# Kernel tuning notes

Measured on AMD Instinct MI355X. Metric: run time of the kernel, lower is better.

## Reference

```python
import jax, jax.numpy as jnp
import numpy as np

B, OBS, H, N = 16384, 512, 1024, 9

def setup_inputs() -> dict:
    key = jax.random.key(0)
    ks = jax.random.split(key, 12)
    s = 0.02
    return {
        "obs": jax.random.normal(ks[0], (B, OBS), jnp.float32),
        "agent_positions": jax.random.normal(ks[1], (B, N, 3), jnp.float32),
        "W1": jax.random.normal(ks[2], (OBS, H), jnp.float32) * s,
        "b1": jnp.zeros((H,), jnp.float32),
        "W2": jax.random.normal(ks[3], (H, H), jnp.float32) * s,
        "b2": jnp.zeros((H,), jnp.float32),
        "Wc1": jax.random.normal(ks[4], (H, H // 2), jnp.float32) * s,
        "bc1": jnp.zeros((H // 2,), jnp.float32),
        "Wc2": jax.random.normal(ks[5], (H // 2, 1), jnp.float32) * s,
        "bc2": jnp.zeros((1,), jnp.float32),
        "Wt1": jax.random.normal(ks[6], (H, H // 2), jnp.float32) * s,
        "bt1": jnp.zeros((H // 2,), jnp.float32),
        "Wt2": jax.random.normal(ks[7], (H // 2, 1), jnp.float32) * s,
        "bt2": jnp.zeros((1,), jnp.float32),
        "Wk1": jax.random.normal(ks[8], (2 * H, H), jnp.float32) * s,
        "bk1": jnp.zeros((H,), jnp.float32),
        "Wk2": jax.random.normal(ks[9], (H, 1), jnp.float32) * s,
        "bk2": jnp.zeros((1,), jnp.float32),
    }


def reference(obs, agent_positions, W1, b1, W2, b2, Wc1, bc1, Wc2, bc2,
              Wt1, bt1, Wt2, bt2, Wk1, bk1, Wk2, bk2):
    # global features: Linear->ReLU->Linear->ReLU
    g = jax.nn.relu(obs @ W1 + b1)
    g = jax.nn.relu(g @ W2 + b2)  # [B, H]

    # Each per-agent head is applied to the SAME g in the original loop,
    # so one pass + broadcast is mathematically identical.
    cov = jax.nn.sigmoid(jax.nn.relu(g @ Wc1 + bc1) @ Wc2 + bc2)  # [B,1]
    trk = jax.nn.sigmoid(jax.nn.relu(g @ Wt1 + bt1) @ Wt2 + bt2)  # [B,1]
    coop_in = jnp.concatenate([g, g], axis=-1)                    # [B,2H]
    coop = jax.nn.sigmoid(jax.nn.relu(coop_in @ Wk1 + bk1) @ Wk2 + bk2)  # [B,1]
    # mean over 8 identical cooperation scores == the score itself

    coverage = jnp.broadcast_to(cov, (cov.shape[0], N))      # [B, N]
    tracking = jnp.broadcast_to(trk, (trk.shape[0], N))      # [B, N]
    cooperation = jnp.broadcast_to(coop, (coop.shape[0], N)) # [B, N]
    return (coverage, tracking, cooperation)
```

## Files before the change

kernel.cpp:

```cpp
#include <hip/hip_runtime.h>
#include <hip/hip_bf16.h>

#define B_ROWS 16384
#define OBS_D  512
#define H_D    1024
#define N_AG   9

typedef __attribute__((ext_vector_type(8))) short short8;
typedef __attribute__((ext_vector_type(4))) float floatx4;

__device__ __forceinline__ unsigned short f_to_bf_raw(float f) {
  union { float f; unsigned u; } c; c.f = f;
  unsigned u = c.u;
  u = u + 0x7FFF + ((u >> 16) & 1);
  return (unsigned short)(u >> 16);
}

__device__ __forceinline__ size_t frag_off(int n, int k, int KT32) {
  const int ft = (n >> 4) * KT32 + (k >> 5);
  const int ln = (n & 15) | (((k >> 3) & 3) << 4);
  return ((size_t)ft * 64 + ln) * 8 + (k & 7);
}

__global__ __launch_bounds__(256) void prep_all(
    const float* __restrict__ obs,
    const float* __restrict__ W1, const float* __restrict__ W2,
    const float* __restrict__ Wc1, const float* __restrict__ Wt1,
    const float* __restrict__ Wk1,
    const float* __restrict__ bc1, const float* __restrict__ bt1,
    const float* __restrict__ bk1,
    const float* __restrict__ Wc2, const float* __restrict__ Wt2,
    const float* __restrict__ Wk2,
    unsigned short* __restrict__ obs_bf,
    unsigned short* __restrict__ W1f, unsigned short* __restrict__ W2f,
    unsigned short* __restrict__ WHf,
    float* __restrict__ bias2048, float* __restrict__ w2cat) {
  __shared__ float t[32][33];
  const int bx  = blockIdx.x;
  const int tid = threadIdx.x;

  if (bx < 4096) {
    int i = (bx * 256 + tid) * 8;
    float4 a = *(const float4*)(obs + i);
    float4 b = *(const float4*)(obs + i + 4);
    short8 o;
    o[0] = (short)f_to_bf_raw(a.x); o[1] = (short)f_to_bf_raw(a.y);
    o[2] = (short)f_to_bf_raw(a.z); o[3] = (short)f_to_bf_raw(a.w);
    o[4] = (short)f_to_bf_raw(b.x); o[5] = (short)f_to_bf_raw(b.y);
    o[6] = (short)f_to_bf_raw(b.z); o[7] = (short)f_to_bf_raw(b.w);
    *(short8*)(obs_bf + i) = o;
    return;
  }

  const int tx = tid & 31;
  const int ty = tid >> 5;

  if (bx < 4608) {
    const int tt = bx - 4096;
    const int k0 = (tt & 15) * 32;
    const int n0 = (tt >> 4) * 32;
#pragma unroll
    for (int i = ty; i < 32; i += 8)
      t[i][tx] = W1[(size_t)(k0 + i) * 1024 + n0 + tx];
    __syncthreads();
#pragma unroll
    for (int i = ty; i < 32; i += 8)
      W1f[frag_off(n0 + i, k0 + tx, 16)] = f_to_bf_raw(t[tx][i]);
    return;
  }

  if (bx < 5632) {
    const int tt = bx - 4608;
    const int k0 = (tt & 31) * 32;
    const int n0 = (tt >> 5) * 32;
#pragma unroll
    for (int i = ty; i < 32; i += 8)
      t[i][tx] = W2[(size_t)(k0 + i) * 1024 + n0 + tx];
    __syncthreads();
#pragma unroll
    for (int i = ty; i < 32; i += 8)
      W2f[frag_off(n0 + i, k0 + tx, 32)] = f_to_bf_raw(t[tx][i]);
    return;
  }

  if (bx < 7680) {
    const int tt = bx - 5632;
    const int k0 = (tt & 31) * 32;
    const int n0 = (tt >> 5) * 32;
#pragma unroll
    for (int i = ty; i < 32; i += 8) {
      const int n = n0 + tx;
      float v;
      if (n0 < 512)
        v = Wc1[(size_t)(k0 + i) * 512 + n];
      else if (n0 < 1024)
        v = Wt1[(size_t)(k0 + i) * 512 + (n - 512)];
      else
        v = Wk1[(size_t)(k0 + i) * 1024 + (n - 1024)]
          + Wk1[(size_t)(k0 + i + 1024) * 1024 + (n - 1024)];
      t[i][tx] = v;
    }
    __syncthreads();
#pragma unroll
    for (int i = ty; i < 32; i += 8)
      WHf[frag_off(n0 + i, k0 + tx, 32)] = f_to_bf_raw(t[tx][i]);
    return;
  }

  {
    int n = (bx - 7680) * 256 + tid;
    float b, w;
    if (n < 512)       { b = bc1[n];        w = Wc2[n]; }
    else if (n < 1024) { b = bt1[n - 512];  w = Wt2[n - 512]; }
    else               { b = bk1[n - 1024]; w = Wk2[n - 1024]; }
    bias2048[n] = b;
    w2cat[n] = w;
  }
}

#define GLD_LDS(gp, lp)                                                        \
  __builtin_amdgcn_global_load_lds(                                            \
      (const __attribute__((address_space(1))) void*)(gp),                     \
      (__attribute__((address_space(3))) void*)(lp), 16, 0, 0)

#define SCB __builtin_amdgcn_sched_barrier(0)

#define MFMA_BF16(a, b, c) __builtin_amdgcn_mfma_f32_16x16x32_bf16(a, b, c, 0, 0, 0)

#define ST_A(T, kh)                                                            \
  GLD_LDS(gA0 + (size_t)(T) * 128 + (kh) * 64,                                 \
          Lds + ((T) & 1) * 65536 + (kh) * 16384 + lA0);                       \
  GLD_LDS(gA1 + (size_t)(T) * 128 + (kh) * 64,                                 \
          Lds + ((T) & 1) * 65536 + (kh) * 16384 + lA0 + 8192)

#define ST_B(T, kh)                                                            \
  GLD_LDS(gB0 + (size_t)(2 * (T) + (kh)) * 1024,                               \
          Lds + ((T) & 1) * 65536 + (kh) * 16384 + lB0);                       \
  GLD_LDS(gB1 + (size_t)(2 * (T) + (kh)) * 1024,                               \
          Lds + ((T) & 1) * 65536 + (kh) * 16384 + lB0 + 8192)

#define FB4(pb)                                                                \
  Fb[0] = *(const short8*)((pb) + fbB);                                        \
  Fb[1] = *(const short8*)((pb) + fbB + 1024);                                 \
  Fb[2] = *(const short8*)((pb) + fbB + 2048);                                 \
  Fb[3] = *(const short8*)((pb) + fbB + 3072)

#define MFMA16(mh)                                                             \
  acc[(mh)*4+0][0] = MFMA_BF16(Fa0, Fb[0], acc[(mh)*4+0][0]);                  \
  acc[(mh)*4+0][1] = MFMA_BF16(Fa0, Fb[1], acc[(mh)*4+0][1]);                  \
  acc[(mh)*4+0][2] = MFMA_BF16(Fa0, Fb[2], acc[(mh)*4+0][2]);                  \
  acc[(mh)*4+0][3] = MFMA_BF16(Fa0, Fb[3], acc[(mh)*4+0][3]);                  \
  acc[(mh)*4+1][0] = MFMA_BF16(Fa1, Fb[0], acc[(mh)*4+1][0]);                  \
  acc[(mh)*4+1][1] = MFMA_BF16(Fa1, Fb[1], acc[(mh)*4+1][1]);                  \
  acc[(mh)*4+1][2] = MFMA_BF16(Fa1, Fb[2], acc[(mh)*4+1][2]);                  \
  acc[(mh)*4+1][3] = MFMA_BF16(Fa1, Fb[3], acc[(mh)*4+1][3]);                  \
  acc[(mh)*4+2][0] = MFMA_BF16(Fa2, Fb[0], acc[(mh)*4+2][0]);                  \
  acc[(mh)*4+2][1] = MFMA_BF16(Fa2, Fb[1], acc[(mh)*4+2][1]);                  \
  acc[(mh)*4+2][2] = MFMA_BF16(Fa2, Fb[2], acc[(mh)*4+2][2]);                  \
  acc[(mh)*4+2][3] = MFMA_BF16(Fa2, Fb[3], acc[(mh)*4+2][3]);                  \
  acc[(mh)*4+3][0] = MFMA_BF16(Fa3, Fb[0], acc[(mh)*4+3][0]);                  \
  acc[(mh)*4+3][1] = MFMA_BF16(Fa3, Fb[1], acc[(mh)*4+3][1]);                  \
  acc[(mh)*4+3][2] = MFMA_BF16(Fa3, Fb[2], acc[(mh)*4+3][2]);                  \
  acc[(mh)*4+3][3] = MFMA_BF16(Fa3, Fb[3], acc[(mh)*4+3][3])

#define PHASE(TT, ks, mh, EXTRA_READS, STAGE_STMT, PRE_BAR2)                   \
  {                                                                            \
    const char* pb = Lds + ((TT) & 1) * 65536 + (ks) * 16384;                  \
    short8 Fa0 = *(const short8*)(pb + faB + ((mh)*4+0)*1024);                 \
    short8 Fa1 = *(const short8*)(pb + faB + ((mh)*4+1)*1024);                 \
    short8 Fa2 = *(const short8*)(pb + faB + ((mh)*4+2)*1024);                 \
    short8 Fa3 = *(const short8*)(pb + faB + ((mh)*4+3)*1024);                 \
    EXTRA_READS;                                                               \
    STAGE_STMT;                                                                \
    SCB; __builtin_amdgcn_s_barrier(); SCB;                                    \
    __builtin_amdgcn_s_setprio(1);                                             \
    MFMA16(mh);                                                                \
    __builtin_amdgcn_s_setprio(0);                                             \
    PRE_BAR2;                                                                  \
    SCB; __builtin_amdgcn_s_barrier(); SCB;                                    \
  }

#define GEMM_CORE_V13(ACC_DECL)                                                \
  __shared__ __align__(16) char Lds[131072];                                   \
  const int tid  = threadIdx.x;                                                \
  const int lane = tid & 63;                                                   \
  const int wave = tid >> 6;                                         \
  const int m0 = blockIdx.x * 256;                                             \
  const int n0 = blockIdx.y * 256;                                             \
  const int wm = (wave & 1) * 128;                  \
  const int wn = (wave >> 1) * 64;                                             \
  const int fr = lane & 15;                                                    \
  const int fq = lane >> 4;                                                    \
  ACC_DECL;                                                                    \
  constexpr int KT   = K >> 6;                                                 \
  constexpr int KT32 = K >> 5;                                                 \
  const size_t rowb = (size_t)K * 2;                                           \
    \
    \
   \
  const char* gA0 = (const char*)A                                             \
      + (size_t)(m0 + wave * 16 + (lane >> 2)) * rowb                          \
      + (((lane & 3) ^ ((lane >> 3) & 3)) * 16);                               \
  const char* gA1 = gA0 + (size_t)128 * rowb;                                  \
  const char* gB0 = (const char*)Bf                                            \
      + ((size_t)((n0 >> 4) + wave) * KT32) * 1024 + lane * 16;                \
  const char* gB1 = gB0 + (size_t)8 * KT32 * 1024;                             \
  const int lA0 = wave * 1024 + lane * 16;                                     \
  const int lB0 = 32768 + wave * 1024 + lane * 16;                             \
       \
  const int faB = (wm + fr) * 64 + ((fq ^ ((fr >> 1) & 3)) * 16);              \
  const int fbB = 32768 + ((wave >> 1) * 4) * 1024 + lane * 16;                \
  short8 Fb[4];                                                                \
              \
  ST_A(0, 0); ST_B(0, 0); ST_A(0, 1); ST_B(0, 1);                              \
  SCB;                                                                         \
  ST_A(1, 0); ST_B(1, 0);                                                      \
  SCB;                                                                         \
  asm volatile("s_waitcnt vmcnt(4)" ::: "memory");       \
  __builtin_amdgcn_s_barrier();                  \
  SCB;                                                                         \
  _Pragma("unroll")                                                            \
  for (int T = 0; T < KT; ++T) {           \
    PHASE(T, 0, 0, FB4(pb), if (T + 1 < KT) { ST_A(T + 1, 1); }, (void)0);     \
    PHASE(T, 0, 1, (void)0, if (T + 1 < KT) { ST_B(T + 1, 1); }, (void)0);     \
    PHASE(T, 1, 0, FB4(pb), if (T + 2 < KT) { ST_A(T + 2, 0); }, (void)0);     \
    PHASE(T, 1, 1, (void)0, if (T + 2 < KT) { ST_B(T + 2, 0); },               \
          if (T + 1 < KT) {                                                    \
            SCB;                                                               \
            if (T + 2 < KT) {                                                  \
              asm volatile("s_waitcnt vmcnt(4)" ::: "memory");                 \
            } else {                                                           \
              asm volatile("s_waitcnt vmcnt(0)" ::: "memory");                 \
            }                                                                  \
            SCB;                                                               \
          });                                                                  \
  }

#define ACC_INIT                                                               \
  floatx4 acc[8][4];                                                           \
  _Pragma("unroll")                                                            \
  for (int i = 0; i < 8; ++i)                                                  \
    _Pragma("unroll")                                                          \
    for (int j = 0; j < 4; ++j) acc[i][j] = (floatx4){0.f, 0.f, 0.f, 0.f}

template <int K>
__global__ __launch_bounds__(512, 2) void gemm_bias_relu(
    const unsigned short* __restrict__ A,
    const unsigned short* __restrict__ Bf,
    const float* __restrict__ bias,
    unsigned short* __restrict__ C,
    int M, int N) {
  GEMM_CORE_V13(ACC_INIT)

#pragma unroll
  for (int ni = 0; ni < 4; ++ni) {
    const int gn = n0 + wn + ni * 16 + fr;
    const float bv = bias[gn];
#pragma unroll
    for (int mi = 0; mi < 8; ++mi) {
#pragma unroll
      for (int r = 0; r < 4; ++r) {
        const int gm = m0 + wm + mi * 16 + fq * 4 + r;
        float v = acc[mi][ni][r] + bv;
        v = v > 0.f ? v : 0.f;
        C[(size_t)gm * N + gn] = f_to_bf_raw(v);
      }
    }
  }
}

template <int K>
__global__ __launch_bounds__(512, 2) void gemm_heads_fused(
    const unsigned short* __restrict__ A,
    const unsigned short* __restrict__ Bf,
    const float* __restrict__ bias,
    const float* __restrict__ w2,
    float* __restrict__ part,
    int M, int N) {
  GEMM_CORE_V13(ACC_INIT)

  const int j = blockIdx.y * 4 + (wave >> 1);
  float w2v[4], bv[4];
#pragma unroll
  for (int ni = 0; ni < 4; ++ni) {
    const int gn = n0 + wn + ni * 16 + fr;
    w2v[ni] = w2[gn];
    bv[ni]  = bias[gn];
  }
#pragma unroll
  for (int mi = 0; mi < 8; ++mi) {
#pragma unroll
    for (int r = 0; r < 4; ++r) {
      float p = 0.f;
#pragma unroll
      for (int ni = 0; ni < 4; ++ni) {
        float v = acc[mi][ni][r] + bv[ni];
        v = v > 0.f ? v : 0.f;
        p += v * w2v[ni];
      }
      p += __shfl_xor(p, 1);
      p += __shfl_xor(p, 2);
      p += __shfl_xor(p, 4);
      p += __shfl_xor(p, 8);
      if (fr == 0) {
        const int gm = m0 + wm + mi * 16 + fq * 4 + r;
        part[(size_t)j * B_ROWS + gm] = p;
      }
    }
  }
}

__global__ __launch_bounds__(256) void final_out(
    const float* __restrict__ part,
    const float* __restrict__ bc2, const float* __restrict__ bt2,
    const float* __restrict__ bk2, float* __restrict__ out) {
  const int row = blockIdx.x * 256 + threadIdx.x;
  float sc = 0.f, st = 0.f, sk = 0.f;
#pragma unroll
  for (int j = 0; j < 8; ++j)  sc += part[(size_t)j * B_ROWS + row];
#pragma unroll
  for (int j = 8; j < 16; ++j) st += part[(size_t)j * B_ROWS + row];
#pragma unroll
  for (int j = 16; j < 32; ++j) sk += part[(size_t)j * B_ROWS + row];
  const float cv = 1.f / (1.f + expf(-(sc + bc2[0])));
  const float tv = 1.f / (1.f + expf(-(st + bt2[0])));
  const float kv = 1.f / (1.f + expf(-(sk + bk2[0])));
  float* o0 = out + (size_t)row * N_AG;
  float* o1 = out + (size_t)(B_ROWS + row) * N_AG;
  float* o2 = out + (size_t)(2 * B_ROWS + row) * N_AG;
#pragma unroll
  for (int a = 0; a < N_AG; ++a) { o0[a] = cv; o1[a] = tv; o2[a] = kv; }
}

extern "C" void kernel_launch(void* const* d_in, const int* in_sizes, int n_in,
                              void* d_out, int out_size, void* d_ws, size_t ws_size,
                              hipStream_t stream) {
  const float* obs = (const float*)d_in[0];
  const float* W1  = (const float*)d_in[2];
  const float* b1  = (const float*)d_in[3];
  const float* W2  = (const float*)d_in[4];
  const float* b2  = (const float*)d_in[5];
  const float* Wc1 = (const float*)d_in[6];
  const float* bc1 = (const float*)d_in[7];
  const float* Wc2 = (const float*)d_in[8];
  const float* bc2 = (const float*)d_in[9];
  const float* Wt1 = (const float*)d_in[10];
  const float* bt1 = (const float*)d_in[11];
  const float* Wt2 = (const float*)d_in[12];
  const float* bt2 = (const float*)d_in[13];
  const float* Wk1 = (const float*)d_in[14];
  const float* bk1 = (const float*)d_in[15];
  const float* Wk2 = (const float*)d_in[16];
  const float* bk2 = (const float*)d_in[17];
  float* out = (float*)d_out;

  char* ws = (char*)d_ws;
  const size_t MB = 1024 * 1024;
  const size_t FULL_NEED = 70 * MB + 16 * 1024;

  unsigned short *obs_bf, *W1f, *W2f, *WHf, *G1, *G;
  float *bias2048, *w2cat, *PART;
  const bool full = (ws_size == 0) || (ws_size >= FULL_NEED);

  if (full) {
    obs_bf   = (unsigned short*)(ws + 0);
    W1f      = (unsigned short*)(ws + 16 * MB);
    G        = (unsigned short*)(ws + 0);
    G1       = (unsigned short*)(ws + 32 * MB);
    PART     = (float*)(ws + 32 * MB);
    W2f      = (unsigned short*)(ws + 64 * MB);
    WHf      = (unsigned short*)(ws + 66 * MB);
    bias2048 = (float*)(ws + 70 * MB);
    w2cat    = (float*)(ws + 70 * MB + 8 * 1024);
  } else {
    obs_bf   = (unsigned short*)(ws + 0);
    G1       = (unsigned short*)(ws + 16 * MB);
    G        = (unsigned short*)(ws + 32 * MB);
    W1f      = (unsigned short*)(ws + 48 * MB);
    W2f      = (unsigned short*)(ws + 49 * MB);
    WHf      = (unsigned short*)(ws + 51 * MB);
    bias2048 = (float*)(ws + 55 * MB);
    w2cat    = (float*)(ws + 55 * MB + 8 * 1024);
    PART     = (float*)(ws + 55 * MB + 16 * 1024);
  }

  prep_all<<<7688, 256, 0, stream>>>(obs, W1, W2, Wc1, Wt1, Wk1,
                                     bc1, bt1, bk1, Wc2, Wt2, Wk2,
                                     obs_bf, W1f, W2f, WHf, bias2048, w2cat);

  if (full) {
    gemm_bias_relu<512><<<dim3(64, 4), 512, 0, stream>>>(
        obs_bf, W1f, b1, G1, B_ROWS, 1024);
    gemm_bias_relu<1024><<<dim3(64, 4), 512, 0, stream>>>(
        G1, W2f, b2, G, B_ROWS, 1024);
    gemm_heads_fused<1024><<<dim3(64, 8), 512, 0, stream>>>(
        G, WHf, bias2048, w2cat, PART, B_ROWS, 2048);
  } else {
    for (int h = 0; h < 2; ++h) {
      const size_t ro = (size_t)h * 8192;
      gemm_bias_relu<512><<<dim3(32, 4), 512, 0, stream>>>(
          obs_bf + ro * 512, W1f, b1, G1, 8192, 1024);
      gemm_bias_relu<1024><<<dim3(32, 4), 512, 0, stream>>>(
          G1, W2f, b2, G, 8192, 1024);
      gemm_heads_fused<1024><<<dim3(32, 8), 512, 0, stream>>>(
          G, WHf, bias2048, w2cat, PART + ro, 8192, 2048);
    }
  }

  final_out<<<B_ROWS / 256, 256, 0, stream>>>(PART, bc2, bt2, bk2, out);
}
```

Measured before the change: 251.8 us.

## Load B fragments directly from global into registers, halve LDS footprint

The weight operand B is no longer staged through LDS. Each wave now reads its pre-swizzled B fragments straight from global memory into registers, double-buffered across k-halves. LDS shrinks from 128KB to 64KB and holds only the A tiles, which cuts LDS write/read traffic and could allow more occupancy. The cost is redundant global/L2 reads of B by the two waves that share the same N columns, and exposed global latency on the B loads. The vmcnt accounting also changes and now mixes register loads with LDS DMA loads.

```diff
diff --git a/kernel.cpp b/kernel.cpp
--- a/kernel.cpp
+++ b/kernel.cpp
@@ -127,61 +127,54 @@
 
 #define MFMA_BF16(a, b, c) __builtin_amdgcn_mfma_f32_16x16x32_bf16(a, b, c, 0, 0, 0)
 
-#define ST_A(T, kh)                                                            \
+#define ST_A14(T, kh)                                                          \
   GLD_LDS(gA0 + (size_t)(T) * 128 + (kh) * 64,                                 \
-          Lds + ((T) & 1) * 65536 + (kh) * 16384 + lA0);                       \
+          Lds + ((T) & 1) * 32768 + (kh) * 16384 + lA0);                       \
   GLD_LDS(gA1 + (size_t)(T) * 128 + (kh) * 64,                                 \
-          Lds + ((T) & 1) * 65536 + (kh) * 16384 + lA0 + 8192)
-
-#define ST_B(T, kh)                                                            \
-  GLD_LDS(gB0 + (size_t)(2 * (T) + (kh)) * 1024,                               \
-          Lds + ((T) & 1) * 65536 + (kh) * 16384 + lB0);                       \
-  GLD_LDS(gB1 + (size_t)(2 * (T) + (kh)) * 1024,                               \
-          Lds + ((T) & 1) * 65536 + (kh) * 16384 + lB0 + 8192)
-
-#define FB4(pb)                                                                \
-  Fb[0] = *(const short8*)((pb) + fbB);                                        \
-  Fb[1] = *(const short8*)((pb) + fbB + 1024);                                 \
-  Fb[2] = *(const short8*)((pb) + fbB + 2048);                                 \
-  Fb[3] = *(const short8*)((pb) + fbB + 3072)
-
-#define MFMA16(mh)                                                             \
-  acc[(mh)*4+0][0] = MFMA_BF16(Fa0, Fb[0], acc[(mh)*4+0][0]);                  \
-  acc[(mh)*4+0][1] = MFMA_BF16(Fa0, Fb[1], acc[(mh)*4+0][1]);                  \
-  acc[(mh)*4+0][2] = MFMA_BF16(Fa0, Fb[2], acc[(mh)*4+0][2]);                  \
-  acc[(mh)*4+0][3] = MFMA_BF16(Fa0, Fb[3], acc[(mh)*4+0][3]);                  \
-  acc[(mh)*4+1][0] = MFMA_BF16(Fa1, Fb[0], acc[(mh)*4+1][0]);                  \
-  acc[(mh)*4+1][1] = MFMA_BF16(Fa1, Fb[1], acc[(mh)*4+1][1]);                  \
-  acc[(mh)*4+1][2] = MFMA_BF16(Fa1, Fb[2], acc[(mh)*4+1][2]);                  \
-  acc[(mh)*4+1][3] = MFMA_BF16(Fa1, Fb[3], acc[(mh)*4+1][3]);                  \
-  acc[(mh)*4+2][0] = MFMA_BF16(Fa2, Fb[0], acc[(mh)*4+2][0]);                  \
-  acc[(mh)*4+2][1] = MFMA_BF16(Fa2, Fb[1], acc[(mh)*4+2][1]);                  \
-  acc[(mh)*4+2][2] = MFMA_BF16(Fa2, Fb[2], acc[(mh)*4+2][2]);                  \
-  acc[(mh)*4+2][3] = MFMA_BF16(Fa2, Fb[3], acc[(mh)*4+2][3]);                  \
-  acc[(mh)*4+3][0] = MFMA_BF16(Fa3, Fb[0], acc[(mh)*4+3][0]);                  \
-  acc[(mh)*4+3][1] = MFMA_BF16(Fa3, Fb[1], acc[(mh)*4+3][1]);                  \
-  acc[(mh)*4+3][2] = MFMA_BF16(Fa3, Fb[2], acc[(mh)*4+3][2]);                  \
-  acc[(mh)*4+3][3] = MFMA_BF16(Fa3, Fb[3], acc[(mh)*4+3][3])
-
-#define PHASE(TT, ks, mh, EXTRA_READS, STAGE_STMT, PRE_BAR2)                   \
+          Lds + ((T) & 1) * 32768 + (kh) * 16384 + lA0 + 8192)
+
+#define LDB(dst, T2, s)                                                        \
+  dst[0] = *(const short8*)(gB + ((size_t)0 * KT32 + 2 * (T2) + (s)) * 512);   \
+  dst[1] = *(const short8*)(gB + ((size_t)1 * KT32 + 2 * (T2) + (s)) * 512);   \
+  dst[2] = *(const short8*)(gB + ((size_t)2 * KT32 + 2 * (T2) + (s)) * 512);   \
+  dst[3] = *(const short8*)(gB + ((size_t)3 * KT32 + 2 * (T2) + (s)) * 512)
+
+#define MFMA16F(mh, FB)                                                        \
+  acc[(mh)*4+0][0] = MFMA_BF16(Fa0, FB[0], acc[(mh)*4+0][0]);                  \
+  acc[(mh)*4+0][1] = MFMA_BF16(Fa0, FB[1], acc[(mh)*4+0][1]);                  \
+  acc[(mh)*4+0][2] = MFMA_BF16(Fa0, FB[2], acc[(mh)*4+0][2]);                  \
+  acc[(mh)*4+0][3] = MFMA_BF16(Fa0, FB[3], acc[(mh)*4+0][3]);                  \
+  acc[(mh)*4+1][0] = MFMA_BF16(Fa1, FB[0], acc[(mh)*4+1][0]);                  \
+  acc[(mh)*4+1][1] = MFMA_BF16(Fa1, FB[1], acc[(mh)*4+1][1]);                  \
+  acc[(mh)*4+1][2] = MFMA_BF16(Fa1, FB[2], acc[(mh)*4+1][2]);                  \
+  acc[(mh)*4+1][3] = MFMA_BF16(Fa1, FB[3], acc[(mh)*4+1][3]);                  \
+  acc[(mh)*4+2][0] = MFMA_BF16(Fa2, FB[0], acc[(mh)*4+2][0]);                  \
+  acc[(mh)*4+2][1] = MFMA_BF16(Fa2, FB[1], acc[(mh)*4+2][1]);                  \
+  acc[(mh)*4+2][2] = MFMA_BF16(Fa2, FB[2], acc[(mh)*4+2][2]);                  \
+  acc[(mh)*4+2][3] = MFMA_BF16(Fa2, FB[3], acc[(mh)*4+2][3]);                  \
+  acc[(mh)*4+3][0] = MFMA_BF16(Fa3, FB[0], acc[(mh)*4+3][0]);                  \
+  acc[(mh)*4+3][1] = MFMA_BF16(Fa3, FB[1], acc[(mh)*4+3][1]);                  \
+  acc[(mh)*4+3][2] = MFMA_BF16(Fa3, FB[2], acc[(mh)*4+3][2]);                  \
+  acc[(mh)*4+3][3] = MFMA_BF16(Fa3, FB[3], acc[(mh)*4+3][3])
+
+#define PHASE14(TT, ks, mh, FB, EXTRA, PRE_BAR2)                               \
   {                                                                            \
-    const char* pb = Lds + ((TT) & 1) * 65536 + (ks) * 16384;                  \
+    const char* pb = Lds + ((TT) & 1) * 32768 + (ks) * 16384;                  \
     short8 Fa0 = *(const short8*)(pb + faB + ((mh)*4+0)*1024);                 \
     short8 Fa1 = *(const short8*)(pb + faB + ((mh)*4+1)*1024);                 \
     short8 Fa2 = *(const short8*)(pb + faB + ((mh)*4+2)*1024);                 \
     short8 Fa3 = *(const short8*)(pb + faB + ((mh)*4+3)*1024);                 \
-    EXTRA_READS;                                                               \
-    STAGE_STMT;                                                                \
+    EXTRA;                                                                     \
     SCB; __builtin_amdgcn_s_barrier(); SCB;                                    \
     __builtin_amdgcn_s_setprio(1);                                             \
-    MFMA16(mh);                                                                \
+    MFMA16F(mh, FB);                                                           \
     __builtin_amdgcn_s_setprio(0);                                             \
     PRE_BAR2;                                                                  \
     SCB; __builtin_amdgcn_s_barrier(); SCB;                                    \
   }
 
-#define GEMM_CORE_V13(ACC_DECL)                                                \
-  __shared__ __align__(16) char Lds[131072];                                   \
+#define GEMM_CORE_V14(ACC_DECL)                                                \
+  __shared__ __align__(16) char Lds[65536];                                    \
   const int tid  = threadIdx.x;                                                \
   const int lane = tid & 63;                                                   \
   const int wave = tid >> 6;                                         \
@@ -195,45 +188,43 @@
   constexpr int KT   = K >> 6;                                                 \
   constexpr int KT32 = K >> 5;                                                 \
   const size_t rowb = (size_t)K * 2;                                           \
-    \
-    \
-   \
+          \
   const char* gA0 = (const char*)A                                             \
       + (size_t)(m0 + wave * 16 + (lane >> 2)) * rowb                          \
       + (((lane & 3) ^ ((lane >> 3) & 3)) * 16);                               \
   const char* gA1 = gA0 + (size_t)128 * rowb;                                  \
-  const char* gB0 = (const char*)Bf                                            \
-      + ((size_t)((n0 >> 4) + wave) * KT32) * 1024 + lane * 16;                \
-  const char* gB1 = gB0 + (size_t)8 * KT32 * 1024;                             \
+              \
+  const unsigned short* gB =                                                   \
+      Bf + ((size_t)(((n0 + wn) >> 4) * KT32) * 64 + lane) * 8;                \
   const int lA0 = wave * 1024 + lane * 16;                                     \
-  const int lB0 = 32768 + wave * 1024 + lane * 16;                             \
-       \
   const int faB = (wm + fr) * 64 + ((fq ^ ((fr >> 1) & 3)) * 16);              \
-  const int fbB = 32768 + ((wave >> 1) * 4) * 1024 + lane * 16;                \
-  short8 Fb[4];                                                                \
-              \
-  ST_A(0, 0); ST_B(0, 0); ST_A(0, 1); ST_B(0, 1);                              \
+  short8 Fb0[4], Fb1[4];                                                       \
+     \
+                                           \
+  ST_A14(0, 0); ST_A14(0, 1);                                                  \
   SCB;                                                                         \
-  ST_A(1, 0); ST_B(1, 0);                                                      \
+  LDB(Fb0, 0, 0);                                                              \
   SCB;                                                                         \
-  asm volatile("s_waitcnt vmcnt(4)" ::: "memory");       \
-  __builtin_amdgcn_s_barrier();                  \
+  asm volatile("s_waitcnt vmcnt(4)" ::: "memory");                             \
+  __builtin_amdgcn_s_barrier();                                                \
   SCB;                                                                         \
   _Pragma("unroll")                                                            \
   for (int T = 0; T < KT; ++T) {           \
-    PHASE(T, 0, 0, FB4(pb), if (T + 1 < KT) { ST_A(T + 1, 1); }, (void)0);     \
-    PHASE(T, 0, 1, (void)0, if (T + 1 < KT) { ST_B(T + 1, 1); }, (void)0);     \
-    PHASE(T, 1, 0, FB4(pb), if (T + 2 < KT) { ST_A(T + 2, 0); }, (void)0);     \
-    PHASE(T, 1, 1, (void)0, if (T + 2 < KT) { ST_B(T + 2, 0); },               \
-          if (T + 1 < KT) {                                                    \
-            SCB;                                                               \
-            if (T + 2 < KT) {                                                  \
+    PHASE14(T, 0, 0, Fb0,                                                      \
+            { LDB(Fb1, T, 1); if (T + 1 < KT) { ST_A14(T + 1, 0); } },         \
+            (void)0);                                                          \
+    PHASE14(T, 0, 1, Fb0,                                                      \
+            { if (T + 1 < KT) { ST_A14(T + 1, 1); } },                         \
+            (void)0);                                                          \
+    PHASE14(T, 1, 0, Fb1,                                                      \
+            { if (T + 1 < KT) { LDB(Fb0, T + 1, 0); } },                       \
+            (void)0);                                                          \
+    PHASE14(T, 1, 1, Fb1, (void)0,                                             \
+            if (T + 1 < KT) {                                                  \
+              SCB;                                                             \
               asm volatile("s_waitcnt vmcnt(4)" ::: "memory");                 \
-            } else {                                                           \
-              asm volatile("s_waitcnt vmcnt(0)" ::: "memory");                 \
-            }                                                                  \
-            SCB;                                                               \
-          });                                                                  \
+              SCB;                                                             \
+            });                                                                \
   }
 
 #define ACC_INIT                                                               \
@@ -250,7 +241,7 @@
     const float* __restrict__ bias,
     unsigned short* __restrict__ C,
     int M, int N) {
-  GEMM_CORE_V13(ACC_INIT)
+  GEMM_CORE_V14(ACC_INIT)
 
 #pragma unroll
   for (int ni = 0; ni < 4; ++ni) {
@@ -277,7 +268,7 @@
     const float* __restrict__ w2,
     float* __restrict__ part,
     int M, int N) {
-  GEMM_CORE_V13(ACC_INIT)
+  GEMM_CORE_V14(ACC_INIT)
 
   const int j = blockIdx.y * 4 + (wave >> 1);
   float w2v[4], bv[4];
```

Result: slower. 272.6 us (+8.3%).
